# Kernel optimization log

Measured on AMD Instinct MI355X. Metric: run time of the kernel, lower is better.

Reference implementation:

```python
import jax, jax.numpy as jnp
import numpy as np
from math import sqrt

N, I, H, O = 2048, 16, 32, 32
CUTS = 8
RADIUS = 9.0
GROUPS = 4
EPS = 1e-5


def leaky(x):
    return jnp.where(x >= 0, x, 0.2 * x)


def group_norm(x, gamma, beta):
    # x: (N, C). Torch applies GroupNorm(4, C) on (1, C, N):
    # normalize over (channels-in-group, N) jointly.
    n, c = x.shape
    xt = x.T.reshape(GROUPS, (c // GROUPS) * n)          # (G, C/G * N)
    mu = xt.mean(axis=1, keepdims=True)
    var = xt.var(axis=1, keepdims=True)
    xn = ((xt - mu) / jnp.sqrt(var + EPS)).reshape(c, n)
    return (xn * gamma[:, None] + beta[:, None]).T       # (N, C)


def setup_inputs() -> dict:
    key = jax.random.key(0)
    ks = jax.random.split(key, 20)
    inp = {
        "points": jax.random.normal(ks[0], (N, 3), jnp.float32) * 5.0,
        "nuv": jax.random.normal(ks[1], (N, 3, 3), jnp.float32),
        "features": jax.random.normal(ks[2], (N, I), jnp.float32),
        # net_in: Linear(I,H), Linear(H,H)
        "W_in1": jax.random.normal(ks[3], (H, I), jnp.float32) / np.sqrt(I),
        "b_in1": jax.random.normal(ks[4], (H,), jnp.float32) * 0.01,
        "W_in2": jax.random.normal(ks[5], (H, H), jnp.float32) / np.sqrt(H),
        "b_in2": jax.random.normal(ks[6], (H,), jnp.float32) * 0.01,
        "g_in_w": jnp.ones((H,), jnp.float32),
        "g_in_b": jnp.zeros((H,), jnp.float32),
        # conv: Linear(3, CUTS), Linear(CUTS, H) with custom init
        "A1": jax.random.normal(ks[7], (CUTS, 3), jnp.float32),
        "A2": jax.random.uniform(ks[9], (H, CUTS), jnp.float32,
                                 minval=-1.0 / np.sqrt(CUTS), maxval=1.0 / np.sqrt(CUTS)),
        # net_out: Linear(H,O), Linear(O,O)
        "W_out1": jax.random.normal(ks[11], (O, H), jnp.float32) / np.sqrt(H),
        "b_out1": jax.random.normal(ks[12], (O,), jnp.float32) * 0.01,
        "W_out2": jax.random.normal(ks[13], (O, O), jnp.float32) / np.sqrt(O),
        "b_out2": jax.random.normal(ks[14], (O,), jnp.float32) * 0.01,
        "g_out_w": jnp.ones((O,), jnp.float32),
        "g_out_b": jnp.zeros((O,), jnp.float32),
    }
    inp["B1"] = (jax.random.uniform(ks[8], (CUTS,), jnp.float32)
                 * 0.8 * jnp.sqrt((inp["A1"] ** 2).sum(-1)))
    inp["B2"] = (jax.random.normal(ks[10], (H,), jnp.float32)
                 * 0.5 * jnp.sqrt((inp["A2"] ** 2).sum(-1)))
    return inp


def reference(points, nuv, features,
              W_in1, b_in1, W_in2, b_in2, g_in_w, g_in_b,
              A1, B1, A2, B2,
              W_out1, b_out1, W_out2, b_out2, g_out_w, g_out_b):
    # 1) net_in + GroupNorm on (1, H, N)
    f = leaky(features @ W_in1.T + b_in1)
    f = leaky(f @ W_in2.T + b_in2)
    f = group_norm(f, g_in_w, g_in_b)                    # (N, H)

    # 2) quasi-geodesic all-pairs interaction
    pts = points / (sqrt(2.0) * RADIUS)
    normals = jax.lax.stop_gradient(nuv[:, 0, :])        # (N, 3), detached
    diff = pts[None, :, :] - pts[:, None, :]             # (N, N, 3) = x_j - x_i
    sq_dist = (diff ** 2).sum(-1)                        # (N, N)
    dot_nn = normals @ normals.T                         # (N, N)
    window = jnp.exp(-sq_dist * (2.0 - dot_nn) ** 2)     # (N, N)

    X_ij = jnp.einsum('iac,ijc->ija', nuv, diff)         # (N, N, 3) local coords
    Xc = jax.nn.relu(jnp.einsum('ijk,ck->ijc', X_ij, A1) + B1)   # (N, N, CUTS)
    Xc = jax.nn.relu(jnp.einsum('ijc,hc->ijh', Xc, A2) + B2)     # (N, N, H)

    F_ij = window[:, :, None] * Xc * f[None, :, :]       # (N, N, H)
    f = F_ij.sum(axis=1)                                 # (N, H)

    # 3) net_out + GroupNorm
    f = leaky(f @ W_out1.T + b_out1)
    f = leaky(f @ W_out2.T + b_out2)
    return group_norm(f, g_out_w, g_out_b)               # (N, O)
```

## Files before the change

### kernel.cpp

```cpp
#include <hip/hip_runtime.h>
#include <hip/hip_bf16.h>

#define NPTS   2048
#define IDIM   16
#define HDIM   32
#define CUTSN  8
#define EPSV   1e-5f
#define PSCALE 0.07856742013183862f

typedef __bf16 bf16x8 __attribute__((ext_vector_type(8)));
typedef float  f32x16 __attribute__((ext_vector_type(16)));

__device__ __forceinline__ float leaky(float x) { return x >= 0.f ? x : 0.2f * x; }

template <int K>
__global__ __launch_bounds__(256) void net2_kernel(
    const float* __restrict__ xin,
    const float* __restrict__ W1, const float* __restrict__ b1,
    const float* __restrict__ W2, const float* __restrict__ b2,
    float* __restrict__ out, float* __restrict__ partials,
    float* __restrict__ zbuf)
{
    const int t = threadIdx.x;
    const int i = blockIdx.x * 256 + t;
    if (zbuf) {
#pragma unroll
        for (int e = 0; e < 8; ++e)
            *(float4*)&zbuf[i * HDIM + e * 4] = make_float4(0.f, 0.f, 0.f, 0.f);
    }
    float x[K];
#pragma unroll
    for (int k = 0; k < K; ++k) x[k] = xin[i * K + k];

    float y[HDIM];
#pragma unroll
    for (int h = 0; h < HDIM; ++h) {
        float v = b1[h];
#pragma unroll
        for (int k = 0; k < K; ++k) v = fmaf(x[k], W1[h * K + k], v);
        y[h] = leaky(v);
    }
    float ps[4]  = {0.f, 0.f, 0.f, 0.f};
    float pss[4] = {0.f, 0.f, 0.f, 0.f};
#pragma unroll
    for (int h = 0; h < HDIM; ++h) {
        float v = b2[h];
#pragma unroll
        for (int k = 0; k < HDIM; ++k) v = fmaf(y[k], W2[h * HDIM + k], v);
        v = leaky(v);
        out[i * HDIM + h] = v;
        const int g = h >> 3;
        ps[g] += v; pss[g] = fmaf(v, v, pss[g]);
    }
#pragma unroll
    for (int off = 32; off; off >>= 1) {
#pragma unroll
        for (int g = 0; g < 4; ++g) {
            ps[g]  += __shfl_down(ps[g],  off, 64);
            pss[g] += __shfl_down(pss[g], off, 64);
        }
    }
    __shared__ float lred[4][8];
    const int wv = t >> 6, ln = t & 63;
    if (ln == 0) {
#pragma unroll
        for (int g = 0; g < 4; ++g) { lred[wv][g] = ps[g]; lred[wv][4 + g] = pss[g]; }
    }
    __syncthreads();
    if (t < 8) {
        const float v = lred[0][t] + lred[1][t] + lred[2][t] + lred[3][t];
        partials[t * 8 + blockIdx.x] = v;
    }
}

__global__ __launch_bounds__(256) void gn_apply_kernel(
    const float* __restrict__ x, const float* __restrict__ partials,
    const float* __restrict__ gw, const float* __restrict__ gb,
    float* __restrict__ out)
{
    const int idx = blockIdx.x * 256 + threadIdx.x;
    const int c = idx & (HDIM - 1);
    const int g = c >> 3;
    float s = 0.f, q = 0.f;
#pragma unroll
    for (int b = 0; b < 8; ++b) {
        s += partials[g * 8 + b];
        q += partials[32 + g * 8 + b];
    }
    const float inv = 1.f / (8.f * NPTS);
    const float mu = s * inv;
    const float rs = rsqrtf(q * inv - mu * mu + EPSV);
    out[idx] = fmaf((x[idx] - mu) * rs, gw[c], gb[c]);
}

__global__ __launch_bounds__(512, 1) void pairwise_kernel(
    const float* __restrict__ points, const float* __restrict__ nuv,
    const float* __restrict__ A1, const float* __restrict__ B1,
    const float* __restrict__ A2, const float* __restrict__ B2,
    const float* __restrict__ traw, const float* __restrict__ partials,
    const float* __restrict__ gw, const float* __restrict__ gb,
    float* __restrict__ fout)
{
    const int t     = threadIdx.x;
    const int lane  = t & 63;
    const int wave  = __builtin_amdgcn_readfirstlane(t >> 6);
    const int h     = lane & 31;
    const int khalf = lane >> 5;
    const int ibase = blockIdx.y * 32;
    const int jt0   = blockIdx.x * 256 + wave * 32;

    __shared__ __align__(16) float4 sIM[32][8];
    __shared__ __align__(16) float  sIP[32][8];
    __shared__ float sacc[32][32];

    if (t < 256) {
        const int il = t >> 3, c = t & 7;
        const int i = ibase + il;
        float m0 = 0.f, m1 = 0.f, m2 = 0.f;
#pragma unroll
        for (int a = 0; a < 3; ++a) {
            const float wA = A1[c * 3 + a];
            m0 = fmaf(wA, nuv[i * 9 + a * 3 + 0], m0);
            m1 = fmaf(wA, nuv[i * 9 + a * 3 + 1], m1);
            m2 = fmaf(wA, nuv[i * 9 + a * 3 + 2], m2);
        }
        sIM[il][c] = make_float4(m0, m1, m2, B1[c]);
    }
    if (t < 32) {
        const int i = ibase + t;
        sIP[t][0] = points[i * 3 + 0] * PSCALE;
        sIP[t][1] = points[i * 3 + 1] * PSCALE;
        sIP[t][2] = points[i * 3 + 2] * PSCALE;
        sIP[t][3] = nuv[i * 9 + 0];
        sIP[t][4] = nuv[i * 9 + 1];
        sIP[t][5] = nuv[i * 9 + 2];
        sIP[t][6] = 0.f; sIP[t][7] = 0.f;
    }
    ((float*)sacc)[t]       = 0.f;
    ((float*)sacc)[t + 512] = 0.f;

    const int j = jt0 + h;
    const float pjx = points[j * 3 + 0] * PSCALE;
    const float pjy = points[j * 3 + 1] * PSCALE;
    const float pjz = points[j * 3 + 2] * PSCALE;
    const float njx = nuv[j * 9 + 0], njy = nuv[j * 9 + 1], njz = nuv[j * 9 + 2];

    bf16x8 bfrag;
#pragma unroll
    for (int e = 0; e < 8; ++e) {
        const float bv = (khalf == 0) ? A2[h * 8 + e] : (e == 0 ? B2[h] : 0.f);
        bfrag[e] = (__bf16)bv;
    }

    const int g4 = h >> 3;
    float s = 0.f, q = 0.f;
#pragma unroll
    for (int b = 0; b < 8; ++b) {
        s += partials[g4 * 8 + b];
        q += partials[32 + g4 * 8 + b];
    }
    const float inv = 1.f / (8.f * NPTS);
    const float mu = s * inv;
    const float rs = rsqrtf(q * inv - mu * mu + EPSV);
    const float alpha = rs * gw[h];
    const float gamma = fmaf(-mu, alpha, gb[h]);
    float freg[16];
#pragma unroll
    for (int r = 0; r < 16; ++r) {
        const int jr = (r & 3) + 8 * (r >> 2) + 4 * khalf;
        freg[r] = fmaf(traw[(jt0 + jr) * HDIM + h], alpha, gamma);
    }

    f32x16 czero;
#pragma unroll
    for (int e = 0; e < 16; ++e) czero[e] = 0.f;

    __syncthreads();

#pragma unroll 1
    for (int il = 0; il < 32; ++il) {
        const float4 ip0 = *(const float4*)&sIP[il][0];
        const float4 ip1 = *(const float4*)&sIP[il][4];
        const float dx = pjx - ip0.x, dy = pjy - ip0.y, dz = pjz - ip0.z;
        const float sq = fmaf(dx, dx, fmaf(dy, dy, dz * dz));
        const float dt = fmaf(ip0.w, njx, fmaf(ip1.x, njy, ip1.y * njz));
        const float tt = 2.f - dt;
        const float wv = __expf(-sq * tt * tt);

        float u[8];
#pragma unroll
        for (int c = 0; c < 8; ++c) {
            const float4 m = sIM[il][c];
            const float cut = fmaf(m.x, dx, fmaf(m.y, dy, fmaf(m.z, dz, m.w)));
            u[c] = wv * fmaxf(cut, 0.f);
        }
        bf16x8 afrag;
        afrag[0] = (__bf16)(khalf == 0 ? u[0] : wv);
#pragma unroll
        for (int e = 1; e < 8; ++e)
            afrag[e] = (__bf16)(khalf == 0 ? u[e] : 0.f);

        const f32x16 d = __builtin_amdgcn_mfma_f32_32x32x16_bf16(
            afrag, bfrag, czero, 0, 0, 0);

        float p0 = 0.f, p1 = 0.f;
#pragma unroll
        for (int r = 0; r < 16; r += 2) {
            p0 = fmaf(fmaxf(d[r],     0.f), freg[r],     p0);
            p1 = fmaf(fmaxf(d[r + 1], 0.f), freg[r + 1], p1);
        }
        atomicAdd(&sacc[il][h], p0 + p1);
    }

    __syncthreads();

    {
        const int cell = t * 2;
        const int il0 = cell >> 5, h0 = cell & 31;
        atomicAdd(&fout[(ibase + il0) * HDIM + h0],     sacc[il0][h0]);
        atomicAdd(&fout[(ibase + il0) * HDIM + h0 + 1], sacc[il0][h0 + 1]);
    }
}

extern "C" void kernel_launch(void* const* d_in, const int* in_sizes, int n_in,
                              void* d_out, int out_size, void* d_ws, size_t ws_size,
                              hipStream_t stream)
{
    const float* points   = (const float*)d_in[0];
    const float* nuv      = (const float*)d_in[1];
    const float* features = (const float*)d_in[2];
    const float* W_in1    = (const float*)d_in[3];
    const float* b_in1    = (const float*)d_in[4];
    const float* W_in2    = (const float*)d_in[5];
    const float* b_in2    = (const float*)d_in[6];
    const float* g_in_w   = (const float*)d_in[7];
    const float* g_in_b   = (const float*)d_in[8];
    const float* A1       = (const float*)d_in[9];
    const float* A2       = (const float*)d_in[10];
    const float* W_out1   = (const float*)d_in[11];
    const float* b_out1   = (const float*)d_in[12];
    const float* W_out2   = (const float*)d_in[13];
    const float* b_out2   = (const float*)d_in[14];
    const float* g_out_w  = (const float*)d_in[15];
    const float* g_out_b  = (const float*)d_in[16];
    const float* B1       = (const float*)d_in[17];
    const float* B2       = (const float*)d_in[18];

    float* ws    = (float*)d_ws;
    float* t2a   = ws;
    float* t2b   = ws + 65536;
    float* fout  = ws + 131072;
    float* part1 = ws + 196608;
    float* part2 = ws + 196672;
    float* out   = (float*)d_out;

    net2_kernel<IDIM><<<dim3(NPTS / 256), dim3(256), 0, stream>>>(
        features, W_in1, b_in1, W_in2, b_in2, t2a, part1, fout);

    pairwise_kernel<<<dim3(NPTS / 256, NPTS / 32), dim3(512), 0, stream>>>(
        points, nuv, A1, B1, A2, B2, t2a, part1, g_in_w, g_in_b, fout);

    net2_kernel<HDIM><<<dim3(NPTS / 256), dim3(256), 0, stream>>>(
        fout, W_out1, b_out1, W_out2, b_out2, t2b, part2, nullptr);
    gn_apply_kernel<<<dim3(NPTS * HDIM / 256), dim3(256), 0, stream>>>(
        t2b, part2, g_out_w, g_out_b, out);
}
```

Before: 185.7 us.

## Precompute per-point pack, halve i-chunk, double-buffer global loads in pairwise

Per-i cut matrices and point/normal data are now computed once in the first MLP kernel and stored as a 48-float pack in workspace. The pairwise kernel drops its shared-memory setup and reads these packs straight from global memory, double-buffered in registers so the load for the next i overlaps compute on the current one. The i-chunk per block shrinks from 32 to 16, which doubles the grid and the number of global atomic flushes to fout. This trades LDS setup and a barrier for uniform global/scalar loads and more register pressure.

```diff
diff --git a/kernel.cpp b/kernel.cpp
--- a/kernel.cpp
+++ b/kernel.cpp
@@ -7,6 +7,8 @@
 #define CUTSN  8
 #define EPSV   1e-5f
 #define PSCALE 0.07856742013183862f
+#define ICH    16
+#define IPK    48
 
 typedef __bf16 bf16x8 __attribute__((ext_vector_type(8)));
 typedef float  f32x16 __attribute__((ext_vector_type(16)));
@@ -19,7 +21,10 @@
     const float* __restrict__ W1, const float* __restrict__ b1,
     const float* __restrict__ W2, const float* __restrict__ b2,
     float* __restrict__ out, float* __restrict__ partials,
-    float* __restrict__ zbuf)
+    float* __restrict__ zbuf,
+    const float* __restrict__ points, const float* __restrict__ nuv,
+    const float* __restrict__ A1, const float* __restrict__ B1,
+    float* __restrict__ ipack)
 {
     const int t = threadIdx.x;
     const int i = blockIdx.x * 256 + t;
@@ -28,6 +33,29 @@
         for (int e = 0; e < 8; ++e)
             *(float4*)&zbuf[i * HDIM + e * 4] = make_float4(0.f, 0.f, 0.f, 0.f);
     }
+    if (ipack) {
+        float* ip = ipack + i * IPK;
+#pragma unroll
+        for (int c = 0; c < 8; ++c) {
+            float m0 = 0.f, m1 = 0.f, m2 = 0.f;
+#pragma unroll
+            for (int a = 0; a < 3; ++a) {
+                const float wA = A1[c * 3 + a];
+                m0 = fmaf(wA, nuv[i * 9 + a * 3 + 0], m0);
+                m1 = fmaf(wA, nuv[i * 9 + a * 3 + 1], m1);
+                m2 = fmaf(wA, nuv[i * 9 + a * 3 + 2], m2);
+            }
+            *(float4*)&ip[c * 4] = make_float4(m0, m1, m2, B1[c]);
+        }
+        *(float4*)&ip[32] = make_float4(points[i * 3 + 0] * PSCALE,
+                                        points[i * 3 + 1] * PSCALE,
+                                        points[i * 3 + 2] * PSCALE,
+                                        nuv[i * 9 + 0]);
+        *(float4*)&ip[36] = make_float4(nuv[i * 9 + 1], nuv[i * 9 + 2], 0.f, 0.f);
+        *(float4*)&ip[40] = make_float4(0.f, 0.f, 0.f, 0.f);
+        *(float4*)&ip[44] = make_float4(0.f, 0.f, 0.f, 0.f);
+    }
+
     float x[K];
 #pragma unroll
     for (int k = 0; k < K; ++k) x[k] = xin[i * K + k];
@@ -95,8 +123,8 @@
 
 __global__ __launch_bounds__(512, 1) void pairwise_kernel(
     const float* __restrict__ points, const float* __restrict__ nuv,
-    const float* __restrict__ A1, const float* __restrict__ B1,
     const float* __restrict__ A2, const float* __restrict__ B2,
+    const float* __restrict__ ipack,
     const float* __restrict__ traw, const float* __restrict__ partials,
     const float* __restrict__ gw, const float* __restrict__ gb,
     float* __restrict__ fout)
@@ -106,38 +134,11 @@
     const int wave  = __builtin_amdgcn_readfirstlane(t >> 6);
     const int h     = lane & 31;
     const int khalf = lane >> 5;
-    const int ibase = blockIdx.y * 32;
+    const int ibase = blockIdx.y * ICH;
     const int jt0   = blockIdx.x * 256 + wave * 32;
 
-    __shared__ __align__(16) float4 sIM[32][8];
-    __shared__ __align__(16) float  sIP[32][8];
-    __shared__ float sacc[32][32];
-
-    if (t < 256) {
-        const int il = t >> 3, c = t & 7;
-        const int i = ibase + il;
-        float m0 = 0.f, m1 = 0.f, m2 = 0.f;
-#pragma unroll
-        for (int a = 0; a < 3; ++a) {
-            const float wA = A1[c * 3 + a];
-            m0 = fmaf(wA, nuv[i * 9 + a * 3 + 0], m0);
-            m1 = fmaf(wA, nuv[i * 9 + a * 3 + 1], m1);
-            m2 = fmaf(wA, nuv[i * 9 + a * 3 + 2], m2);
-        }
-        sIM[il][c] = make_float4(m0, m1, m2, B1[c]);
-    }
-    if (t < 32) {
-        const int i = ibase + t;
-        sIP[t][0] = points[i * 3 + 0] * PSCALE;
-        sIP[t][1] = points[i * 3 + 1] * PSCALE;
-        sIP[t][2] = points[i * 3 + 2] * PSCALE;
-        sIP[t][3] = nuv[i * 9 + 0];
-        sIP[t][4] = nuv[i * 9 + 1];
-        sIP[t][5] = nuv[i * 9 + 2];
-        sIP[t][6] = 0.f; sIP[t][7] = 0.f;
-    }
-    ((float*)sacc)[t]       = 0.f;
-    ((float*)sacc)[t + 512] = 0.f;
+    __shared__ float sacc[ICH][32];
+    if (t < ICH * 32) ((float*)sacc)[t] = 0.f;
 
     const int j = jt0 + h;
     const float pjx = points[j * 3 + 0] * PSCALE;
@@ -177,48 +178,61 @@
 
     __syncthreads();
 
+#define LOADI(M, G0, G1, il) do {                                             \
+        const float4* ip4 = (const float4*)(ipack + (ibase + (il)) * IPK);    \
+        M[0] = ip4[0]; M[1] = ip4[1]; M[2] = ip4[2]; M[3] = ip4[3];           \
+        M[4] = ip4[4]; M[5] = ip4[5]; M[6] = ip4[6]; M[7] = ip4[7];           \
+        G0 = ip4[8]; G1 = ip4[9];                                             \
+    } while (0)
+
+#define BODY(M, G0, G1, il) do {                                              \
+        const float dx = pjx - G0.x, dy = pjy - G0.y, dz = pjz - G0.z;        \
+        const float sq = fmaf(dx, dx, fmaf(dy, dy, dz * dz));                 \
+        const float dt = fmaf(G0.w, njx, fmaf(G1.x, njy, G1.y * njz));        \
+        const float tt = 2.f - dt;                                            \
+        const float wv = __expf(-sq * tt * tt);                               \
+        float u[8];                                                           \
+        _Pragma("unroll")                                                     \
+        for (int c = 0; c < 8; ++c) {                                         \
+            const float cut = fmaf(M[c].x, dx, fmaf(M[c].y, dy,               \
+                              fmaf(M[c].z, dz, M[c].w)));                     \
+            u[c] = wv * fmaxf(cut, 0.f);                                      \
+        }                                                                     \
+        bf16x8 afrag;                                                         \
+        afrag[0] = (__bf16)(khalf == 0 ? u[0] : wv);                          \
+        _Pragma("unroll")                                                     \
+        for (int e = 1; e < 8; ++e)                                           \
+            afrag[e] = (__bf16)(khalf == 0 ? u[e] : 0.f);                     \
+        const f32x16 d = __builtin_amdgcn_mfma_f32_32x32x16_bf16(             \
+            afrag, bfrag, czero, 0, 0, 0);                                    \
+        float p0 = 0.f, p1 = 0.f, p2 = 0.f, p3 = 0.f;                         \
+        _Pragma("unroll")                                                     \
+        for (int r = 0; r < 16; r += 4) {                                     \
+            p0 = fmaf(fmaxf(d[r],     0.f), freg[r],     p0);                 \
+            p1 = fmaf(fmaxf(d[r + 1], 0.f), freg[r + 1], p1);                 \
+            p2 = fmaf(fmaxf(d[r + 2], 0.f), freg[r + 2], p2);                 \
+            p3 = fmaf(fmaxf(d[r + 3], 0.f), freg[r + 3], p3);                 \
+        }                                                                     \
+        atomicAdd(&sacc[il][h], (p0 + p1) + (p2 + p3));                       \
+    } while (0)
+
+    float4 MA[8], MB[8], GA0, GA1, GB0, GB1;
+    LOADI(MA, GA0, GA1, 0);
 #pragma unroll 1
-    for (int il = 0; il < 32; ++il) {
-        const float4 ip0 = *(const float4*)&sIP[il][0];
-        const float4 ip1 = *(const float4*)&sIP[il][4];
-        const float dx = pjx - ip0.x, dy = pjy - ip0.y, dz = pjz - ip0.z;
-        const float sq = fmaf(dx, dx, fmaf(dy, dy, dz * dz));
-        const float dt = fmaf(ip0.w, njx, fmaf(ip1.x, njy, ip1.y * njz));
-        const float tt = 2.f - dt;
-        const float wv = __expf(-sq * tt * tt);
-
-        float u[8];
-#pragma unroll
-        for (int c = 0; c < 8; ++c) {
-            const float4 m = sIM[il][c];
-            const float cut = fmaf(m.x, dx, fmaf(m.y, dy, fmaf(m.z, dz, m.w)));
-            u[c] = wv * fmaxf(cut, 0.f);
-        }
-        bf16x8 afrag;
-        afrag[0] = (__bf16)(khalf == 0 ? u[0] : wv);
-#pragma unroll
-        for (int e = 1; e < 8; ++e)
-            afrag[e] = (__bf16)(khalf == 0 ? u[e] : 0.f);
-
-        const f32x16 d = __builtin_amdgcn_mfma_f32_32x32x16_bf16(
-            afrag, bfrag, czero, 0, 0, 0);
-
-        float p0 = 0.f, p1 = 0.f;
-#pragma unroll
-        for (int r = 0; r < 16; r += 2) {
-            p0 = fmaf(fmaxf(d[r],     0.f), freg[r],     p0);
-            p1 = fmaf(fmaxf(d[r + 1], 0.f), freg[r + 1], p1);
-        }
-        atomicAdd(&sacc[il][h], p0 + p1);
-    }
+    for (int ii = 0; ii < ICH; ii += 2) {
+        LOADI(MB, GB0, GB1, ii + 1);
+        BODY(MA, GA0, GA1, ii);
+        if (ii + 2 < ICH) LOADI(MA, GA0, GA1, ii + 2);
+        BODY(MB, GB0, GB1, ii + 1);
+    }
+#undef LOADI
+#undef BODY
 
     __syncthreads();
 
     {
-        const int cell = t * 2;
-        const int il0 = cell >> 5, h0 = cell & 31;
-        atomicAdd(&fout[(ibase + il0) * HDIM + h0],     sacc[il0][h0]);
-        atomicAdd(&fout[(ibase + il0) * HDIM + h0 + 1], sacc[il0][h0 + 1]);
+        const int il0 = t >> 5, h0 = t & 31;
+        atomicAdd(&fout[(ibase + il0) * HDIM + h0], sacc[il0][h0]);
     }
 }
 
@@ -250,18 +264,21 @@
     float* t2a   = ws;
     float* t2b   = ws + 65536;
     float* fout  = ws + 131072;
-    float* part1 = ws + 196608;
-    float* part2 = ws + 196672;
+    float* ipack = ws + 196608;
+    float* part1 = ws + 294912;
+    float* part2 = ws + 294976;
     float* out   = (float*)d_out;
 
     net2_kernel<IDIM><<<dim3(NPTS / 256), dim3(256), 0, stream>>>(
-        features, W_in1, b_in1, W_in2, b_in2, t2a, part1, fout);
-
-    pairwise_kernel<<<dim3(NPTS / 256, NPTS / 32), dim3(512), 0, stream>>>(
-        points, nuv, A1, B1, A2, B2, t2a, part1, g_in_w, g_in_b, fout);
+        features, W_in1, b_in1, W_in2, b_in2, t2a, part1, fout,
+        points, nuv, A1, B1, ipack);
+
+    pairwise_kernel<<<dim3(NPTS / 256, NPTS / ICH), dim3(512), 0, stream>>>(
+        points, nuv, A2, B2, ipack, t2a, part1, g_in_w, g_in_b, fout);
 
     net2_kernel<HDIM><<<dim3(NPTS / 256), dim3(256), 0, stream>>>(
-        fout, W_out1, b_out1, W_out2, b_out2, t2b, part2, nullptr);
+        fout, W_out1, b_out1, W_out2, b_out2, t2b, part2, nullptr,
+        nullptr, nullptr, nullptr, nullptr, nullptr);
     gn_apply_kernel<<<dim3(NPTS * HDIM / 256), dim3(256), 0, stream>>>(
         t2b, part2, g_out_w, g_out_b, out);
 }
```

Result: faster. 178.7 us (-3.8%).
